# Optimization experiments

Hardware: AMD Instinct MI355X
Metric: run time of the kernel (lower is better)

Reference implementation:

```python
import jax, jax.numpy as jnp
import numpy as np

B, C_FEAT, C_COND, C_KEY, H, W = 4, 256, 256, 32, 64, 64


def setup_inputs() -> dict:
    key = jax.random.key(0)
    ks = jax.random.split(key, 8)
    s = 0.02
    return {
        "features": jax.random.normal(ks[0], (B, C_FEAT, H, W), jnp.float32),
        "conditions": jax.random.normal(ks[1], (B, C_COND, H, W), jnp.float32),
        "Wq": jax.random.normal(ks[2], (C_KEY, C_COND), jnp.float32) * s,
        "bq": jnp.zeros((C_KEY,), jnp.float32),
        "Wk": jax.random.normal(ks[3], (C_KEY, C_FEAT), jnp.float32) * s,
        "bk": jnp.zeros((C_KEY,), jnp.float32),
        "Wv": jax.random.normal(ks[4], (C_FEAT, C_FEAT), jnp.float32) * s,
        "bv": jnp.zeros((C_FEAT,), jnp.float32),
        "gamma": jnp.zeros((1,), jnp.float32),
    }


def reference(features, conditions, Wq, bq, Wk, bk, Wv, bv, gamma):
    b, c, h, w = features.shape
    n = h * w
    feat = features.reshape(b, c, n)            # [B, C, N]
    cond = conditions.reshape(b, cond_c := conditions.shape[1], n)
    # 1x1 convs == per-pixel linear projections
    q = jnp.einsum('kc,bcn->bnk', Wq, cond) + bq          # [B, N, Ck]
    k = jnp.einsum('kc,bcn->bkn', Wk, feat) + bk[:, None]  # [B, Ck, N]
    v = jnp.einsum('oc,bcn->bon', Wv, feat) + bv[:, None]  # [B, C, N]
    energy = jnp.einsum('bik,bkj->bij', q, k)             # [B, N, N]
    attn = jax.nn.softmax(energy, axis=-1)
    out = jnp.einsum('bcj,bij->bci', v, attn)             # [B, C, N]
    out = out.reshape(b, c, h, w)
    return gamma * out + features
```

## Files before the change

kernel.cpp:

```cpp
#include <hip/hip_runtime.h>

typedef __bf16 bf16_t;
typedef __bf16 bf16x2 __attribute__((ext_vector_type(2)));
typedef __bf16 bf16x4 __attribute__((ext_vector_type(4)));
typedef __bf16 bf16x8 __attribute__((ext_vector_type(8)));
typedef float f32x4 __attribute__((ext_vector_type(4)));
typedef unsigned u32;
typedef unsigned u32x4 __attribute__((ext_vector_type(4)));

#define N_PIX 4096
#define CFEAT 256
#define CKEY 32
#define NBATCH 4

#if __has_builtin(__builtin_amdgcn_exp2f)
#define EXP2(x) __builtin_amdgcn_exp2f(x)
#else
#define EXP2(x) exp2f(x)
#endif

static __device__ __forceinline__ f32x4 mfma16(bf16x8 a, bf16x8 b, f32x4 c) {
    return __builtin_amdgcn_mfma_f32_16x16x32_bf16(a, b, c, 0, 0, 0);
}

static __device__ __forceinline__ void glds16(const void* g, void* l) {
    __builtin_amdgcn_global_load_lds(
        (const __attribute__((address_space(1))) void*)g,
        (__attribute__((address_space(3))) void*)l, 16, 0, 0);
}

static __device__ __forceinline__ u32 pk2(float lo, float hi) {
    bf16x2 t; t[0] = (bf16_t)lo; t[1] = (bf16_t)hi;
    return __builtin_bit_cast(u32, t);
}

static __device__ __forceinline__ void xpose4(u32 &x, u32 &y) {
#if __has_builtin(__builtin_amdgcn_permlane32_swap) && __has_builtin(__builtin_amdgcn_permlane16_swap)
    auto r32 = __builtin_amdgcn_permlane32_swap(x, y, false, false);
    auto r16 = __builtin_amdgcn_permlane16_swap(r32[0], r32[1], false, false);
    x = r16[0]; y = r16[1];
#else
    const int lane = threadIdx.x & 63;
    const int g = lane >> 4, ln = lane & 15;
    const int i0 = ln + ((g & 1) << 5);
    const int i2 = i0 + 16;
    u32 xs0 = (u32)__shfl((int)x, i0), ys0 = (u32)__shfl((int)y, i0);
    u32 xs2 = (u32)__shfl((int)x, i2), ys2 = (u32)__shfl((int)y, i2);
    x = (g < 2) ? xs0 : ys0;
    y = (g < 2) ? xs2 : ys2;
#endif
}

static __device__ __forceinline__ void softmax_tile(
    const bf16x8 kf[4], bf16x8 qf, bf16x8 ones,
    f32x4 &accsum, bf16x8 &pa0, bf16x8 &pa1)
{
    f32x4 zero = {0.f, 0.f, 0.f, 0.f};
    f32x4 st[4];
#pragma unroll
    for (int jt = 0; jt < 4; ++jt) st[jt] = mfma16(kf[jt], qf, zero);
    float ex[16];
#pragma unroll
    for (int jt = 0; jt < 4; ++jt)
#pragma unroll
        for (int r = 0; r < 4; ++r) ex[jt * 4 + r] = EXP2(st[jt][r]);
    u32 a0 = pk2(ex[0],  ex[1]),  a1 = pk2(ex[2],  ex[3]);
    u32 b0 = pk2(ex[4],  ex[5]),  b1 = pk2(ex[6],  ex[7]);
    u32 c0 = pk2(ex[8],  ex[9]),  c1 = pk2(ex[10], ex[11]);
    u32 d0 = pk2(ex[12], ex[13]), d1 = pk2(ex[14], ex[15]);
    xpose4(a0, b0); xpose4(a1, b1);
    xpose4(c0, d0); xpose4(c1, d1);
    u32x4 w0 = {a0, a1, b0, b1};
    u32x4 w1 = {c0, c1, d0, d1};
    pa0 = __builtin_bit_cast(bf16x8, w0);
    pa1 = __builtin_bit_cast(bf16x8, w1);
    accsum = mfma16(ones, pa0, accsum);
    accsum = mfma16(ones, pa1, accsum);
}

__global__ __launch_bounds__(256) void proj_kernel(
    const float* __restrict__ Wq, const float* __restrict__ bq, const float* __restrict__ cond,
    const float* __restrict__ Wk, const float* __restrict__ bk, const float* __restrict__ feat,
    const float* __restrict__ Wv, const float* __restrict__ bv,
    bf16_t* __restrict__ Qt, bf16_t* __restrict__ Kt, bf16_t* __restrict__ Vv)
{
    __shared__ __attribute__((aligned(16))) bf16_t T[64][40];
    const int lane = threadIdx.x & 63, wave = threadIdx.x >> 6;
    const int g = lane >> 4, ln = lane & 15;
    const int bid = blockIdx.x;
    f32x4 zero = {0.f, 0.f, 0.f, 0.f};

    if (bid < 512) {
        const bool isK = (bid >= 256);
        const int idx = bid & 255;
        const int xt = idx & 63;
        const int b  = idx >> 6;
        const float* W    = isK ? Wk : Wq;
        const float* bias = isK ? bk : bq;
        const float* X  = (isK ? feat : cond) + (size_t)b * CFEAT * N_PIX;
        bf16_t*      Yt = (isK ? Kt : Qt) + (size_t)b * N_PIX * CKEY;
        const float qscale = isK ? 1.0f : 1.4426950408889634f;

        const int m_base = (wave & 1) * 16;
        const int n_loc  = (wave >> 1) * 32;
        const int n_base = xt * 64 + n_loc;

        f32x4 acc[2] = {zero, zero};
        for (int k0 = 0; k0 < CFEAT; k0 += 32) {
            bf16x8 a;
            const float* wp = W + (size_t)(m_base + ln) * CFEAT + k0 + g * 8;
#pragma unroll
            for (int j = 0; j < 8; ++j) a[j] = (bf16_t)wp[j];
#pragma unroll
            for (int nt = 0; nt < 2; ++nt) {
                const float* xp = X + (size_t)(k0 + g * 8) * N_PIX + n_base + nt * 16 + ln;
                bf16x8 bfr;
#pragma unroll
                for (int j = 0; j < 8; ++j) bfr[j] = (bf16_t)xp[(size_t)j * N_PIX];
                acc[nt] = mfma16(a, bfr, acc[nt]);
            }
        }
#pragma unroll
        for (int nt = 0; nt < 2; ++nt)
#pragma unroll
            for (int r = 0; r < 4; ++r) {
                const int ck = m_base + g * 4 + r;
                T[n_loc + nt * 16 + ln][ck] = (bf16_t)((acc[nt][r] + bias[ck]) * qscale);
            }
        __syncthreads();
        const int n  = threadIdx.x >> 2;
        const int sg = threadIdx.x & 3;
        bf16x8 row = *(const bf16x8*)&T[n][sg * 8];
        *(bf16x8*)&Yt[(size_t)(xt * 64 + n) * CKEY + sg * 8] = row;
    } else {
        const int idx = bid - 512;
        const int xt = idx & 127;
        const int b  = idx >> 7;
        const int n_base = xt * 32;
        const int c_wave = wave * 64;
        const float* Xb = feat + (size_t)b * CFEAT * N_PIX;
        bf16_t*      Vb = Vv + (size_t)b * CFEAT * N_PIX;

        f32x4 acc[4][2];
#pragma unroll
        for (int mt = 0; mt < 4; ++mt) { acc[mt][0] = zero; acc[mt][1] = zero; }

        for (int k0 = 0; k0 < CFEAT; k0 += 32) {
            bf16x8 bfr[2];
#pragma unroll
            for (int nt = 0; nt < 2; ++nt) {
                const float* xp = Xb + (size_t)(k0 + g * 8) * N_PIX + n_base + nt * 16 + ln;
#pragma unroll
                for (int j = 0; j < 8; ++j) bfr[nt][j] = (bf16_t)xp[(size_t)j * N_PIX];
            }
#pragma unroll
            for (int mt = 0; mt < 4; ++mt) {
                const float* wp = Wv + (size_t)(c_wave + mt * 16 + ln) * CFEAT + k0 + g * 8;
                bf16x8 a;
#pragma unroll
                for (int j = 0; j < 8; ++j) a[j] = (bf16_t)wp[j];
                acc[mt][0] = mfma16(a, bfr[0], acc[mt][0]);
                acc[mt][1] = mfma16(a, bfr[1], acc[mt][1]);
            }
        }
#pragma unroll
        for (int mt = 0; mt < 4; ++mt)
#pragma unroll
            for (int nt = 0; nt < 2; ++nt)
#pragma unroll
                for (int r = 0; r < 4; ++r) {
                    const int m = c_wave + mt * 16 + g * 4 + r;
                    const int n = n_base + nt * 16 + ln;
                    Vb[(size_t)m * N_PIX + n] = (bf16_t)(acc[mt][nt][r] + bv[m]);
                }
    }
}

__global__ __launch_bounds__(256, 2) void pv_kernel(
    const bf16_t* __restrict__ Qt, const bf16_t* __restrict__ Kt,
    const bf16_t* __restrict__ V,
    const float* __restrict__ features, const float* __restrict__ gamma,
    float* __restrict__ out)
{
    __shared__ __attribute__((aligned(16))) bf16_t Vlds[4][128 * 64];

    const int lane = threadIdx.x & 63, wave = threadIdx.x >> 6;
    const int g = lane >> 4, ln = lane & 15;
    const int b = blockIdx.z;
    const int i_base = blockIdx.y * 64 + wave * 16;
    const int c_base = blockIdx.x * 128;

    const bf16_t* Qb = Qt + (size_t)b * N_PIX * CKEY;
    const bf16_t* Kb = Kt + (size_t)b * N_PIX * CKEY;
    const bf16_t* Vb = V + (size_t)b * CFEAT * N_PIX;

    const int s0 = wave * 256 + lane, s1 = s0 + 64, s2 = s0 + 128, s3 = s0 + 192;
    const int sc0 = s0 >> 3, sj0 = (s0 & 7) ^ (sc0 & 7);
    const int sc1 = s1 >> 3, sj1 = (s1 & 7) ^ (sc1 & 7);
    const int sc2 = s2 >> 3, sj2 = (s2 & 7) ^ (sc2 & 7);
    const int sc3 = s3 >> 3, sj3 = (s3 & 7) ^ (sc3 & 7);
    const bf16_t* vg0 = Vb + (size_t)(c_base + sc0) * N_PIX + sj0 * 8;
    const bf16_t* vg1 = Vb + (size_t)(c_base + sc1) * N_PIX + sj1 * 8;
    const bf16_t* vg2 = Vb + (size_t)(c_base + sc2) * N_PIX + sj2 * 8;
    const bf16_t* vg3 = Vb + (size_t)(c_base + sc3) * N_PIX + sj3 * 8;

    const bf16x8 qf = *(const bf16x8*)&Qb[(size_t)(i_base + ln) * CKEY + g * 8];

    bf16x8 ones;
#pragma unroll
    for (int j = 0; j < 8; ++j) ones[j] = (bf16_t)1.0f;

    f32x4 zero = {0.f, 0.f, 0.f, 0.f};
    f32x4 acc[8] = {zero, zero, zero, zero, zero, zero, zero, zero};
    f32x4 accsum = zero;

    bf16x8 kfA[4], kfB[4];
    bf16x8 pa0c, pa1c;

    {
        bf16x8 kf0[4];
#pragma unroll
        for (int jt = 0; jt < 4; ++jt)
            kf0[jt] = *(const bf16x8*)&Kb[(size_t)(jt * 16 + ln) * CKEY + g * 8];
        asm volatile("" ::: "memory");
        glds16(vg0, &Vlds[0][wave * 2048]);
        glds16(vg1, &Vlds[0][wave * 2048 + 512]);
        glds16(vg2, &Vlds[0][wave * 2048 + 1024]);
        glds16(vg3, &Vlds[0][wave * 2048 + 1536]);
        glds16(vg0 + 64, &Vlds[1][wave * 2048]);
        glds16(vg1 + 64, &Vlds[1][wave * 2048 + 512]);
        glds16(vg2 + 64, &Vlds[1][wave * 2048 + 1024]);
        glds16(vg3 + 64, &Vlds[1][wave * 2048 + 1536]);
#pragma unroll
        for (int jt = 0; jt < 4; ++jt)
            kfA[jt] = *(const bf16x8*)&Kb[(size_t)(64 + jt * 16 + ln) * CKEY + g * 8];
        softmax_tile(kf0, qf, ones, accsum, pa0c, pa1c);
        asm volatile("s_waitcnt vmcnt(8)" ::: "memory");
        __builtin_amdgcn_s_barrier();
        asm volatile("" ::: "memory");
    }

#define PV_ITER(NN, KFU, KFN)                                                  \
  {                                                                            \
    const int nn = (NN);                                                       \
    const bf16_t* Vt = &Vlds[nn & 3][0];                                       \
    bf16x8 vf[16];                                                             \
    _Pragma("unroll")                                                          \
    for (int ct = 0; ct < 8; ++ct) {                                           \
      const int c = ct * 16 + ln;                                              \
      vf[2 * ct]     = *(const bf16x8*)&Vt[(c * 8 + ( g      ^ (c & 7))) * 8]; \
      vf[2 * ct + 1] = *(const bf16x8*)&Vt[(c * 8 + ((4 + g) ^ (c & 7))) * 8]; \
    }                                                                          \
    const int jq2 = ((nn + 2) & 63) * 64;                                      \
    _Pragma("unroll")                                                          \
    for (int jt = 0; jt < 4; ++jt)                                             \
      KFN[jt] = *(const bf16x8*)&Kb[(size_t)(jq2 + jt * 16 + ln) * CKEY + g * 8]; \
    asm volatile("" ::: "memory");     \
    const int jn = (nn * 64 + 128) & (N_PIX - 1);                              \
    bf16_t* ldst = &Vlds[(nn + 2) & 3][wave * 2048];                           \
    glds16(vg0 + jn, ldst);                                                    \
    glds16(vg1 + jn, ldst + 512);                                              \
    glds16(vg2 + jn, ldst + 1024);                                             \
    glds16(vg3 + jn, ldst + 1536);                                             \
    bf16x8 pa0n, pa1n;                                                         \
    const bool live = (nn < 63);                                               \
    if (live) softmax_tile(KFU, qf, ones, accsum, pa0n, pa1n);                 \
    asm volatile("s_waitcnt vmcnt(8)" ::: "memory");                           \
    __builtin_amdgcn_s_barrier();                                              \
    asm volatile("" ::: "memory");                                             \
    __builtin_amdgcn_s_setprio(1);                                             \
    _Pragma("unroll")                                                          \
    for (int ct = 0; ct < 8; ++ct) {                                           \
      acc[ct] = mfma16(vf[2 * ct],     pa0c, acc[ct]);                         \
      acc[ct] = mfma16(vf[2 * ct + 1], pa1c, acc[ct]);                         \
    }                                                                          \
    __builtin_amdgcn_s_setprio(0);                                             \
    if (live) { pa0c = pa0n; pa1c = pa1n; }                                    \
  }

    for (int n2 = 0; n2 < 32; ++n2) {
        PV_ITER(2 * n2,     kfA, kfB);
        PV_ITER(2 * n2 + 1, kfB, kfA);
    }
#undef PV_ITER

    const float s_lane = gamma[0] / accsum[0];

#pragma unroll
    for (int ct = 0; ct < 8; ++ct)
#pragma unroll
        for (int r = 0; r < 4; ++r) {
            const int c = c_base + ct * 16 + g * 4 + r;
            const int i = i_base + ln;
            const size_t idx = ((size_t)b * CFEAT + c) * N_PIX + i;
            out[idx] = s_lane * acc[ct][r] + features[idx];
        }
}

extern "C" void kernel_launch(void* const* d_in, const int* in_sizes, int n_in,
                              void* d_out, int out_size, void* d_ws, size_t ws_size,
                              hipStream_t stream) {
    const float* features   = (const float*)d_in[0];
    const float* conditions = (const float*)d_in[1];
    const float* Wq  = (const float*)d_in[2];
    const float* bq  = (const float*)d_in[3];
    const float* Wk  = (const float*)d_in[4];
    const float* bk  = (const float*)d_in[5];
    const float* Wv  = (const float*)d_in[6];
    const float* bv  = (const float*)d_in[7];
    const float* gam = (const float*)d_in[8];
    float* out = (float*)d_out;

    bf16_t* Qt = (bf16_t*)d_ws;
    bf16_t* Kt = Qt + (size_t)NBATCH * N_PIX * CKEY;
    bf16_t* Vw = Kt + (size_t)NBATCH * N_PIX * CKEY;

    proj_kernel<<<dim3(1024, 1, 1), 256, 0, stream>>>(
        Wq, bq, conditions, Wk, bk, features, Wv, bv, Qt, Kt, Vw);
    pv_kernel<<<dim3(2, N_PIX / 64, NBATCH), 256, 0, stream>>>(
        Qt, Kt, Vw, features, gam, out);
}
```

Before: 169.4 us.

## Pre-transpose inputs to bf16 and give each PV wave two query tiles

Adds a prep kernel that transposes and converts conditions and features to pixel-major bf16, using the output buffer as scratch. The projection kernels can then load contiguous bf16x8 fragments instead of strided scalar fp32 loads, and weights are read with vectorised casts. The PV kernel drops to 128 threads per block, with each wave handling 32 query rows in two tiles, so every V fragment read from LDS feeds twice as many MFMAs and the K prefetch double-buffering is simplified. The cost is an extra kernel launch plus a full read and write of both inputs, more registers per wave in PV, and fewer waves per block.

```diff
diff --git a/kernel.cpp b/kernel.cpp
--- a/kernel.cpp
+++ b/kernel.cpp
@@ -2,10 +2,10 @@
 
 typedef __bf16 bf16_t;
 typedef __bf16 bf16x2 __attribute__((ext_vector_type(2)));
-typedef __bf16 bf16x4 __attribute__((ext_vector_type(4)));
 typedef __bf16 bf16x8 __attribute__((ext_vector_type(8)));
 typedef float f32x4 __attribute__((ext_vector_type(4)));
 typedef unsigned u32;
+typedef unsigned u32x2 __attribute__((ext_vector_type(2)));
 typedef unsigned u32x4 __attribute__((ext_vector_type(4)));
 
 #define N_PIX 4096
@@ -32,6 +32,14 @@
 static __device__ __forceinline__ u32 pk2(float lo, float hi) {
     bf16x2 t; t[0] = (bf16_t)lo; t[1] = (bf16_t)hi;
     return __builtin_bit_cast(u32, t);
+}
+
+static __device__ __forceinline__ bf16x8 cast8(const float* p) {
+    f32x4 lo = *(const f32x4*)p;
+    f32x4 hi = *(const f32x4*)(p + 4);
+    u32x4 w = {pk2(lo[0], lo[1]), pk2(lo[2], lo[3]),
+               pk2(hi[0], hi[1]), pk2(hi[2], hi[3])};
+    return __builtin_bit_cast(bf16x8, w);
 }
 
 static __device__ __forceinline__ void xpose4(u32 &x, u32 &y) {
@@ -78,10 +86,46 @@
     accsum = mfma16(ones, pa1, accsum);
 }
 
+__global__ __launch_bounds__(256) void prep_kernel(
+    const float* __restrict__ cond, const float* __restrict__ feat,
+    bf16_t* __restrict__ XTc, bf16_t* __restrict__ XTf)
+{
+    __shared__ __attribute__((aligned(16))) float T[64][68];
+    const int tid = threadIdx.x, bid = blockIdx.x;
+    const int t = bid >> 10;
+    const int r = bid & 1023;
+    const int b = r >> 8;
+    const int tile = r & 255;
+    const int ct = tile >> 6, nt = tile & 63;
+    const float* src = (t ? feat : cond) +
+                       ((size_t)b * CFEAT + ct * 64) * N_PIX + (size_t)nt * 64;
+    bf16_t* dst = (t ? XTf : XTc) +
+                  ((size_t)b * N_PIX + nt * 64) * CFEAT + ct * 64;
+
+    const int cl = tid >> 4, n4 = (tid & 15) * 4;
+#pragma unroll
+    for (int q = 0; q < 4; ++q) {
+        f32x4 v = *(const f32x4*)&src[(size_t)(cl + q * 16) * N_PIX + n4];
+        *(f32x4*)&T[cl + q * 16][n4] = v;
+    }
+    __syncthreads();
+    const int n_loc = tid >> 2;
+#pragma unroll
+    for (int h = 0; h < 2; ++h) {
+        const int c0 = (tid & 3) * 16 + h * 8;
+        u32x4 o;
+#pragma unroll
+        for (int p = 0; p < 4; ++p)
+            o[p] = pk2(T[c0 + 2 * p][n_loc], T[c0 + 2 * p + 1][n_loc]);
+        *(u32x4*)&dst[(size_t)n_loc * CFEAT + c0] = o;
+    }
+}
+
 __global__ __launch_bounds__(256) void proj_kernel(
-    const float* __restrict__ Wq, const float* __restrict__ bq, const float* __restrict__ cond,
-    const float* __restrict__ Wk, const float* __restrict__ bk, const float* __restrict__ feat,
+    const float* __restrict__ Wq, const float* __restrict__ bq,
+    const float* __restrict__ Wk, const float* __restrict__ bk,
     const float* __restrict__ Wv, const float* __restrict__ bv,
+    const bf16_t* __restrict__ XTc, const bf16_t* __restrict__ XTf,
     bf16_t* __restrict__ Qt, bf16_t* __restrict__ Kt, bf16_t* __restrict__ Vv)
 {
     __shared__ __attribute__((aligned(16))) bf16_t T[64][40];
@@ -97,8 +141,8 @@
         const int b  = idx >> 6;
         const float* W    = isK ? Wk : Wq;
         const float* bias = isK ? bk : bq;
-        const float* X  = (isK ? feat : cond) + (size_t)b * CFEAT * N_PIX;
-        bf16_t*      Yt = (isK ? Kt : Qt) + (size_t)b * N_PIX * CKEY;
+        const bf16_t* XT = (isK ? XTf : XTc) + (size_t)b * N_PIX * CFEAT;
+        bf16_t* Yt = (isK ? Kt : Qt) + (size_t)b * N_PIX * CKEY;
         const float qscale = isK ? 1.0f : 1.4426950408889634f;
 
         const int m_base = (wave & 1) * 16;
@@ -106,17 +150,13 @@
         const int n_base = xt * 64 + n_loc;
 
         f32x4 acc[2] = {zero, zero};
+#pragma unroll
         for (int k0 = 0; k0 < CFEAT; k0 += 32) {
-            bf16x8 a;
-            const float* wp = W + (size_t)(m_base + ln) * CFEAT + k0 + g * 8;
-#pragma unroll
-            for (int j = 0; j < 8; ++j) a[j] = (bf16_t)wp[j];
+            bf16x8 a = cast8(W + (size_t)(m_base + ln) * CFEAT + k0 + g * 8);
 #pragma unroll
             for (int nt = 0; nt < 2; ++nt) {
-                const float* xp = X + (size_t)(k0 + g * 8) * N_PIX + n_base + nt * 16 + ln;
-                bf16x8 bfr;
-#pragma unroll
-                for (int j = 0; j < 8; ++j) bfr[j] = (bf16_t)xp[(size_t)j * N_PIX];
+                bf16x8 bfr = *(const bf16x8*)
+                    &XT[(size_t)(n_base + nt * 16 + ln) * CFEAT + k0 + g * 8];
                 acc[nt] = mfma16(a, bfr, acc[nt]);
             }
         }
@@ -138,27 +178,23 @@
         const int b  = idx >> 7;
         const int n_base = xt * 32;
         const int c_wave = wave * 64;
-        const float* Xb = feat + (size_t)b * CFEAT * N_PIX;
-        bf16_t*      Vb = Vv + (size_t)b * CFEAT * N_PIX;
+        const bf16_t* XT = XTf + (size_t)b * N_PIX * CFEAT;
+        bf16_t* Vb = Vv + (size_t)b * CFEAT * N_PIX;
 
         f32x4 acc[4][2];
 #pragma unroll
         for (int mt = 0; mt < 4; ++mt) { acc[mt][0] = zero; acc[mt][1] = zero; }
 
+#pragma unroll
         for (int k0 = 0; k0 < CFEAT; k0 += 32) {
             bf16x8 bfr[2];
 #pragma unroll
-            for (int nt = 0; nt < 2; ++nt) {
-                const float* xp = Xb + (size_t)(k0 + g * 8) * N_PIX + n_base + nt * 16 + ln;
-#pragma unroll
-                for (int j = 0; j < 8; ++j) bfr[nt][j] = (bf16_t)xp[(size_t)j * N_PIX];
-            }
+            for (int nt = 0; nt < 2; ++nt)
+                bfr[nt] = *(const bf16x8*)
+                    &XT[(size_t)(n_base + nt * 16 + ln) * CFEAT + k0 + g * 8];
 #pragma unroll
             for (int mt = 0; mt < 4; ++mt) {
-                const float* wp = Wv + (size_t)(c_wave + mt * 16 + ln) * CFEAT + k0 + g * 8;
-                bf16x8 a;
-#pragma unroll
-                for (int j = 0; j < 8; ++j) a[j] = (bf16_t)wp[j];
+                bf16x8 a = cast8(Wv + (size_t)(c_wave + mt * 16 + ln) * CFEAT + k0 + g * 8);
                 acc[mt][0] = mfma16(a, bfr[0], acc[mt][0]);
                 acc[mt][1] = mfma16(a, bfr[1], acc[mt][1]);
             }
@@ -176,7 +212,7 @@
     }
 }
 
-__global__ __launch_bounds__(256, 2) void pv_kernel(
+__global__ __launch_bounds__(128, 1) void pv_kernel(
     const bf16_t* __restrict__ Qt, const bf16_t* __restrict__ Kt,
     const bf16_t* __restrict__ V,
     const float* __restrict__ features, const float* __restrict__ gamma,
@@ -187,113 +223,117 @@
     const int lane = threadIdx.x & 63, wave = threadIdx.x >> 6;
     const int g = lane >> 4, ln = lane & 15;
     const int b = blockIdx.z;
-    const int i_base = blockIdx.y * 64 + wave * 16;
+    const int i_base = blockIdx.y * 64 + wave * 32;
     const int c_base = blockIdx.x * 128;
 
     const bf16_t* Qb = Qt + (size_t)b * N_PIX * CKEY;
     const bf16_t* Kb = Kt + (size_t)b * N_PIX * CKEY;
     const bf16_t* Vb = V + (size_t)b * CFEAT * N_PIX;
 
-    const int s0 = wave * 256 + lane, s1 = s0 + 64, s2 = s0 + 128, s3 = s0 + 192;
-    const int sc0 = s0 >> 3, sj0 = (s0 & 7) ^ (sc0 & 7);
-    const int sc1 = s1 >> 3, sj1 = (s1 & 7) ^ (sc1 & 7);
-    const int sc2 = s2 >> 3, sj2 = (s2 & 7) ^ (sc2 & 7);
-    const int sc3 = s3 >> 3, sj3 = (s3 & 7) ^ (sc3 & 7);
-    const bf16_t* vg0 = Vb + (size_t)(c_base + sc0) * N_PIX + sj0 * 8;
-    const bf16_t* vg1 = Vb + (size_t)(c_base + sc1) * N_PIX + sj1 * 8;
-    const bf16_t* vg2 = Vb + (size_t)(c_base + sc2) * N_PIX + sj2 * 8;
-    const bf16_t* vg3 = Vb + (size_t)(c_base + sc3) * N_PIX + sj3 * 8;
-
-    const bf16x8 qf = *(const bf16x8*)&Qb[(size_t)(i_base + ln) * CKEY + g * 8];
+    const bf16_t* vgp[8];
+#pragma unroll
+    for (int q = 0; q < 8; ++q) {
+        const int s = wave * 512 + q * 64 + lane;
+        const int sc = s >> 3, sj = (s & 7) ^ (sc & 7);
+        vgp[q] = Vb + (size_t)(c_base + sc) * N_PIX + sj * 8;
+    }
+
+    const bf16x8 qf0 = *(const bf16x8*)&Qb[(size_t)(i_base + ln) * CKEY + g * 8];
+    const bf16x8 qf1 = *(const bf16x8*)&Qb[(size_t)(i_base + 16 + ln) * CKEY + g * 8];
 
     bf16x8 ones;
 #pragma unroll
     for (int j = 0; j < 8; ++j) ones[j] = (bf16_t)1.0f;
 
     f32x4 zero = {0.f, 0.f, 0.f, 0.f};
-    f32x4 acc[8] = {zero, zero, zero, zero, zero, zero, zero, zero};
-    f32x4 accsum = zero;
-
-    bf16x8 kfA[4], kfB[4];
-    bf16x8 pa0c, pa1c;
+    f32x4 acc[8][2];
+#pragma unroll
+    for (int ct = 0; ct < 8; ++ct) { acc[ct][0] = zero; acc[ct][1] = zero; }
+    f32x4 accsum0 = zero, accsum1 = zero;
+
+    bf16x8 pa0c0, pa1c0, pa0c1, pa1c1;
 
     {
-        bf16x8 kf0[4];
+        bf16x8 kf[4];
 #pragma unroll
         for (int jt = 0; jt < 4; ++jt)
-            kf0[jt] = *(const bf16x8*)&Kb[(size_t)(jt * 16 + ln) * CKEY + g * 8];
+            kf[jt] = *(const bf16x8*)&Kb[(size_t)(jt * 16 + ln) * CKEY + g * 8];
         asm volatile("" ::: "memory");
-        glds16(vg0, &Vlds[0][wave * 2048]);
-        glds16(vg1, &Vlds[0][wave * 2048 + 512]);
-        glds16(vg2, &Vlds[0][wave * 2048 + 1024]);
-        glds16(vg3, &Vlds[0][wave * 2048 + 1536]);
-        glds16(vg0 + 64, &Vlds[1][wave * 2048]);
-        glds16(vg1 + 64, &Vlds[1][wave * 2048 + 512]);
-        glds16(vg2 + 64, &Vlds[1][wave * 2048 + 1024]);
-        glds16(vg3 + 64, &Vlds[1][wave * 2048 + 1536]);
-#pragma unroll
-        for (int jt = 0; jt < 4; ++jt)
-            kfA[jt] = *(const bf16x8*)&Kb[(size_t)(64 + jt * 16 + ln) * CKEY + g * 8];
-        softmax_tile(kf0, qf, ones, accsum, pa0c, pa1c);
+#pragma unroll
+        for (int q = 0; q < 8; ++q)
+            glds16(vgp[q], &Vlds[0][(wave * 512 + q * 64) * 8]);
+#pragma unroll
+        for (int q = 0; q < 8; ++q)
+            glds16(vgp[q] + 64, &Vlds[1][(wave * 512 + q * 64) * 8]);
+        softmax_tile(kf, qf0, ones, accsum0, pa0c0, pa1c0);
+        softmax_tile(kf, qf1, ones, accsum1, pa0c1, pa1c1);
         asm volatile("s_waitcnt vmcnt(8)" ::: "memory");
         __builtin_amdgcn_s_barrier();
         asm volatile("" ::: "memory");
     }
 
-#define PV_ITER(NN, KFU, KFN)                                                  \
-  {                                                                            \
-    const int nn = (NN);                                                       \
-    const bf16_t* Vt = &Vlds[nn & 3][0];                                       \
-    bf16x8 vf[16];                                                             \
-    _Pragma("unroll")                                                          \
-    for (int ct = 0; ct < 8; ++ct) {                                           \
-      const int c = ct * 16 + ln;                                              \
-      vf[2 * ct]     = *(const bf16x8*)&Vt[(c * 8 + ( g      ^ (c & 7))) * 8]; \
-      vf[2 * ct + 1] = *(const bf16x8*)&Vt[(c * 8 + ((4 + g) ^ (c & 7))) * 8]; \
-    }                                                                          \
-    const int jq2 = ((nn + 2) & 63) * 64;                                      \
-    _Pragma("unroll")                                                          \
-    for (int jt = 0; jt < 4; ++jt)                                             \
-      KFN[jt] = *(const bf16x8*)&Kb[(size_t)(jq2 + jt * 16 + ln) * CKEY + g * 8]; \
-    asm volatile("" ::: "memory");     \
-    const int jn = (nn * 64 + 128) & (N_PIX - 1);                              \
-    bf16_t* ldst = &Vlds[(nn + 2) & 3][wave * 2048];                           \
-    glds16(vg0 + jn, ldst);                                                    \
-    glds16(vg1 + jn, ldst + 512);                                              \
-    glds16(vg2 + jn, ldst + 1024);                                             \
-    glds16(vg3 + jn, ldst + 1536);                                             \
-    bf16x8 pa0n, pa1n;                                                         \
-    const bool live = (nn < 63);                                               \
-    if (live) softmax_tile(KFU, qf, ones, accsum, pa0n, pa1n);                 \
-    asm volatile("s_waitcnt vmcnt(8)" ::: "memory");                           \
-    __builtin_amdgcn_s_barrier();                                              \
-    asm volatile("" ::: "memory");                                             \
-    __builtin_amdgcn_s_setprio(1);                                             \
-    _Pragma("unroll")                                                          \
-    for (int ct = 0; ct < 8; ++ct) {                                           \
-      acc[ct] = mfma16(vf[2 * ct],     pa0c, acc[ct]);                         \
-      acc[ct] = mfma16(vf[2 * ct + 1], pa1c, acc[ct]);                         \
-    }                                                                          \
-    __builtin_amdgcn_s_setprio(0);                                             \
-    if (live) { pa0c = pa0n; pa1c = pa1n; }                                    \
-  }
-
-    for (int n2 = 0; n2 < 32; ++n2) {
-        PV_ITER(2 * n2,     kfA, kfB);
-        PV_ITER(2 * n2 + 1, kfB, kfA);
-    }
-#undef PV_ITER
-
-    const float s_lane = gamma[0] / accsum[0];
+    for (int n = 0; n < 64; ++n) {
+        const int jq = ((n + 1) & 63) * 64;
+        bf16x8 kf[4];
+#pragma unroll
+        for (int jt = 0; jt < 4; ++jt)
+            kf[jt] = *(const bf16x8*)&Kb[(size_t)(jq + jt * 16 + ln) * CKEY + g * 8];
+
+        const bf16_t* Vt = &Vlds[n & 3][0];
+        bf16x8 vf[16];
+#pragma unroll
+        for (int ct = 0; ct < 8; ++ct) {
+            const int c = ct * 16 + ln;
+            vf[2 * ct]     = *(const bf16x8*)&Vt[(c * 8 + ( g      ^ (c & 7))) * 8];
+            vf[2 * ct + 1] = *(const bf16x8*)&Vt[(c * 8 + ((4 + g) ^ (c & 7))) * 8];
+        }
+        asm volatile("" ::: "memory");
+
+        const int jn = (n * 64 + 128) & (N_PIX - 1);
+        bf16_t* ldb = &Vlds[(n + 2) & 3][0];
+#pragma unroll
+        for (int q = 0; q < 8; ++q)
+            glds16(vgp[q] + jn, &ldb[(wave * 512 + q * 64) * 8]);
+
+        bf16x8 pa0n0, pa1n0, pa0n1, pa1n1;
+        const bool live = (n < 63);
+        if (live) {
+            softmax_tile(kf, qf0, ones, accsum0, pa0n0, pa1n0);
+            softmax_tile(kf, qf1, ones, accsum1, pa0n1, pa1n1);
+        }
+
+        asm volatile("s_waitcnt vmcnt(8)" ::: "memory");
+        __builtin_amdgcn_s_barrier();
+        asm volatile("" ::: "memory");
+
+        __builtin_amdgcn_s_setprio(1);
+#pragma unroll
+        for (int ct = 0; ct < 8; ++ct) {
+            acc[ct][0] = mfma16(vf[2 * ct],     pa0c0, acc[ct][0]);
+            acc[ct][0] = mfma16(vf[2 * ct + 1], pa1c0, acc[ct][0]);
+            acc[ct][1] = mfma16(vf[2 * ct],     pa0c1, acc[ct][1]);
+            acc[ct][1] = mfma16(vf[2 * ct + 1], pa1c1, acc[ct][1]);
+        }
+        __builtin_amdgcn_s_setprio(0);
+        if (live) {
+            pa0c0 = pa0n0; pa1c0 = pa1n0;
+            pa0c1 = pa0n1; pa1c1 = pa1n1;
+        }
+    }
+
+    const float s0 = gamma[0] / accsum0[0];
+    const float s1 = gamma[0] / accsum1[0];
 
 #pragma unroll
     for (int ct = 0; ct < 8; ++ct)
 #pragma unroll
         for (int r = 0; r < 4; ++r) {
             const int c = c_base + ct * 16 + g * 4 + r;
-            const int i = i_base + ln;
-            const size_t idx = ((size_t)b * CFEAT + c) * N_PIX + i;
-            out[idx] = s_lane * acc[ct][r] + features[idx];
+            const size_t row = ((size_t)b * CFEAT + c) * N_PIX;
+            const size_t idx0 = row + i_base + ln;
+            const size_t idx1 = row + i_base + 16 + ln;
+            out[idx0] = s0 * acc[ct][0][r] + features[idx0];
+            out[idx1] = s1 * acc[ct][1][r] + features[idx1];
         }
 }
 
@@ -314,9 +354,12 @@
     bf16_t* Qt = (bf16_t*)d_ws;
     bf16_t* Kt = Qt + (size_t)NBATCH * N_PIX * CKEY;
     bf16_t* Vw = Kt + (size_t)NBATCH * N_PIX * CKEY;
-
+    bf16_t* XTc = (bf16_t*)d_out;
+    bf16_t* XTf = XTc + (size_t)NBATCH * N_PIX * CFEAT;
+
+    prep_kernel<<<dim3(2048, 1, 1), 256, 0, stream>>>(conditions, features, XTc, XTf);
     proj_kernel<<<dim3(1024, 1, 1), 256, 0, stream>>>(
-        Wq, bq, conditions, Wk, bk, features, Wv, bv, Qt, Kt, Vw);
-    pv_kernel<<<dim3(2, N_PIX / 64, NBATCH), 256, 0, stream>>>(
+        Wq, bq, Wk, bk, Wv, bv, XTc, XTf, Qt, Kt, Vw);
+    pv_kernel<<<dim3(2, N_PIX / 64, NBATCH), 128, 0, stream>>>(
         Qt, Kt, Vw, features, gam, out);
 }
```

Result: slower. 200.9 us (+18.6%).
